# Kernel tuning notes

Hardware: AMD Instinct MI355X
Metric: run time of the kernel (lower is better)

Reference implementation:

```python
import jax, jax.numpy as jnp
import numpy as np

EPS = 1e-5  # torch BatchNorm1d default eps

def _bn(x, g, b):
    # BatchNorm1d in training mode: batch mean, biased variance
    m = jnp.mean(x, axis=0)
    v = jnp.mean((x - m) ** 2, axis=0)
    return g * (x - m) * jax.lax.rsqrt(v + EPS) + b

N_ENT, N_REL = 50000, 200
D_E = D_R = 32
RANK = 32
NI = 1024  # must satisfy NI**2 == D_R * D_E**3
B = 64

def setup_inputs() -> dict:
    key = jax.random.key(0)
    ks = jax.random.split(key, 10)
    s = 0.001
    inp = {
        "E": s * jax.random.normal(ks[0], (N_ENT, D_E), jnp.float32),
        "R": s * jax.random.normal(ks[1], (N_REL, D_R), jnp.float32),
        "U_root": s * jax.random.normal(ks[2], (N_REL, RANK, RANK), jnp.float32),
        "U12": s * jax.random.normal(ks[3], (RANK, NI, NI), jnp.float32),
        "U3R": s * jax.random.normal(ks[4], (RANK, NI, NI), jnp.float32),
        "P": s * jax.random.normal(ks[5], (RANK, D_E), jnp.float32),
        "g_r": jnp.ones((D_R,), jnp.float32), "b_r": jnp.zeros((D_R,), jnp.float32),
        "g_e": jnp.ones((D_E,), jnp.float32), "b_e": jnp.zeros((D_E,), jnp.float32),
        "g_w": jnp.ones((D_E,), jnp.float32), "b_w": jnp.zeros((D_E,), jnp.float32),
        "r_idx": jax.random.randint(ks[6], (B,), 0, N_REL),
        "e2_idx": jax.random.randint(ks[7], (B,), 0, N_ENT),
        "e3_idx": jax.random.randint(ks[8], (B,), 0, N_ENT),
        "miss_ent_domain": 3,
    }
    return inp

def reference(E, R, U_root, U12, U3R, P, g_r, b_r, g_e, b_e, g_w, b_w,
              r_idx, e2_idx, e3_idx, miss_ent_domain):
    Bsz = r_idx.shape[0]
    d_r, d_e = R.shape[1], E.shape[1]

    r_emb = _bn(R[r_idx], g_r, b_r)                      # (B, d_r)

    # einsum 'brs,ria,rjb,rkc->bijk' with P.unsqueeze(1): the dangling
    # indices s, a, b, c are each summed out independently, so the
    # contraction factorizes into rank-1 pieces over r.
    a = U_root[r_idx].sum(-1)                            # (B, r)
    u12 = U12.sum(-1)                                    # (r, ni)
    u3 = U3R.sum(-1)                                     # (r, ni)
    p = P.sum(-1)                                        # (r,)
    W = jnp.einsum('br,ri,rj,r->bij', a, u12, u3, p)     # (B, ni, ni)
    W = W.reshape(Bsz, d_r, d_e, d_e, d_e)               # implicit HT core

    # bmm(r_emb (B,1,d_r), W (B,d_r,-1))
    W_mat = jnp.einsum('bd,bdijk->bijk', r_emb, W)       # (B, d_e, d_e, d_e)

    e2 = _bn(E[e2_idx], g_e, b_e)                        # (B, d_e)
    e3 = _bn(E[e3_idx], g_e, b_e)                        # (B, d_e)

    if miss_ent_domain == 1:
        vec = jnp.einsum('bijk,bk,bj->bi', W_mat, e3, e2)
    elif miss_ent_domain == 2:
        vec = jnp.einsum('bijk,bk,bi->bj', W_mat, e3, e2)
    else:
        vec = jnp.einsum('bijk,bi,bj->bk', W_mat, e2, e3)

    vec = _bn(vec, g_w, b_w)                             # (B, d_e)
    logits = vec @ E.T                                   # (B, |E|)
    return jax.nn.softmax(logits, axis=1)
```

## Files before the change

kernel.cpp:

```cpp
#include <hip/hip_runtime.h>
#include <math.h>

#define NENT 50000
#define DD   32
#define BSZ  64
#define NI   1024
#define NROWS 65536
#define EPS  1e-5f

#define WS_U12S 0
#define WS_U3S  32768
#define WS_P    65536
#define WS_A    65568
#define WS_RE   67616
#define WS_E2   69664
#define WS_E3   71712
#define WS_VEC  73760
#define WS_VECN 75808
#define WS_INV  77856

__device__ void bn_block(const float* __restrict__ src, const int* __restrict__ idx,
                         const float* __restrict__ g, const float* __restrict__ bb,
                         float* __restrict__ dst, float* xs, float* st) {
    for (int i = threadIdx.x; i < BSZ * DD; i += 256) {
        int b = i >> 5, d = i & 31;
        xs[i] = src[(size_t)idx[b] * DD + d];
    }
    __syncthreads();
    if (threadIdx.x < DD) {
        int d = threadIdx.x;
        float m = 0.f;
        for (int b = 0; b < BSZ; ++b) m += xs[b * 32 + d];
        m *= (1.f / 64.f);
        float v = 0.f;
        for (int b = 0; b < BSZ; ++b) { float t = xs[b * 32 + d] - m; v += t * t; }
        v *= (1.f / 64.f);
        st[d]      = m;
        st[32 + d] = g[d] / sqrtf(v + EPS);
    }
    __syncthreads();
    for (int i = threadIdx.x; i < BSZ * DD; i += 256) {
        int d = i & 31;
        dst[i] = (xs[i] - st[d]) * st[32 + d] + bb[d];
    }
    __syncthreads();
}

__global__ __launch_bounds__(256) void k1_rowsums(
    const float* __restrict__ U12, const float* __restrict__ U3R,
    const float* __restrict__ R, const float* __restrict__ E,
    const float* __restrict__ U_root, const float* __restrict__ P,
    const float* __restrict__ g_r, const float* __restrict__ b_r,
    const float* __restrict__ g_e, const float* __restrict__ b_e,
    const int* __restrict__ r_idx, const int* __restrict__ e2_idx,
    const int* __restrict__ e3_idx, float* __restrict__ ws) {
    __shared__ float xs[BSZ * DD];
    __shared__ float st[64];
    int blk = blockIdx.x;
    if (blk < NROWS / 4) {
        int wave = threadIdx.x >> 6, lane = threadIdx.x & 63;
        int row = blk * 4 + wave;
        const float* src = (row < 32768) ? (U12 + (size_t)row * NI)
                                         : (U3R + (size_t)(row - 32768) * NI);
        const float4* p4 = (const float4*)src;
        float s = 0.f;
#pragma unroll
        for (int t = 0; t < 4; ++t) {
            float4 v = p4[t * 64 + lane];
            s += (v.x + v.y) + (v.z + v.w);
        }
#pragma unroll
        for (int o = 32; o; o >>= 1) s += __shfl_down(s, o, 64);
        if (lane == 0) ws[row] = s;
        return;
    }
    int tid = threadIdx.x;
    float* wp   = ws + WS_P;
    float* wa   = ws + WS_A;
    float* wvec = ws + WS_VEC;
    if (tid < 32) {
        float s = 0.f;
#pragma unroll
        for (int c = 0; c < 32; ++c) s += P[tid * 32 + c];
        wp[tid] = s;
    }
    for (int i = tid; i < BSZ * DD; i += 256) {
        int b = i >> 5, r = i & 31;
        const float* u = U_root + (size_t)r_idx[b] * (DD * DD) + r * 32;
        float s = 0.f;
#pragma unroll
        for (int c = 0; c < 32; ++c) s += u[c];
        wa[i]   = s;
        wvec[i] = 0.f;
    }
    bn_block(R, r_idx,  g_r, b_r, ws + WS_RE, xs, st);
    bn_block(E, e2_idx, g_e, b_e, ws + WS_E2, xs, st);
    bn_block(E, e3_idx, g_e, b_e, ws + WS_E3, xs, st);
}

__global__ __launch_bounds__(256) void k2b_core(float* __restrict__ ws) {
    const float* u12s = ws + WS_U12S;
    const float* u3s  = ws + WS_U3S;
    const float* wp   = ws + WS_P;
    const float* wa   = ws + WS_A;
    const float* wre  = ws + WS_RE;
    const float* we2  = ws + WS_E2;
    const float* we3  = ws + WS_E3;
    float* wvec = ws + WS_VEC;
    int lane = threadIdx.x & 63;
    int pair = blockIdx.x * 4 + (threadIdx.x >> 6);
    int b = pair >> 5, r = pair & 31;
    float e2v = we2[b * 32 + (lane & 31)];
    const float* u12r = u12s + r * NI;
    float acc = 0.f;
#pragma unroll
    for (int t = 0; t < 16; ++t) {
        int di = t * 64 + lane;
        acc += u12r[di] * wre[b * 32 + (di >> 5)] * e2v;
    }
#pragma unroll
    for (int o = 32; o; o >>= 1) acc += __shfl_xor(acc, o, 64);
    int k = lane & 31, j0 = (lane >> 5) * 16;
    const float* u3r = u3s + r * NI;
    float bacc = 0.f;
#pragma unroll
    for (int jj = 0; jj < 16; ++jj) {
        int j = j0 + jj;
        bacc += we3[b * 32 + j] * u3r[j * 32 + k];
    }
    bacc += __shfl_down(bacc, 32, 64);
    if (lane < 32) {
        float coef = wa[b * 32 + r] * wp[r] * acc;
        atomicAdd(&wvec[b * 32 + k], coef * bacc);
    }
}

__global__ __launch_bounds__(256) void k2c_bnw(const float* __restrict__ g_w,
                                               const float* __restrict__ b_w,
                                               float* __restrict__ ws) {
    __shared__ float xs[BSZ * DD];
    __shared__ float st[64];
    const float* wvec = ws + WS_VEC;
    float* wvecn = ws + WS_VECN;
    for (int i = threadIdx.x; i < BSZ * DD; i += 256) xs[i] = wvec[i];
    __syncthreads();
    if (threadIdx.x < DD) {
        int d = threadIdx.x;
        float m = 0.f;
        for (int b = 0; b < BSZ; ++b) m += xs[b * 32 + d];
        m *= (1.f / 64.f);
        float v = 0.f;
        for (int b = 0; b < BSZ; ++b) { float t = xs[b * 32 + d] - m; v += t * t; }
        v *= (1.f / 64.f);
        st[d]      = m;
        st[32 + d] = g_w[d] / sqrtf(v + EPS);
    }
    __syncthreads();
    for (int i = threadIdx.x; i < BSZ * DD; i += 256) {
        int d = i & 31;
        wvecn[i] = (xs[i] - st[d]) * st[32 + d] + b_w[d];
    }
}

__global__ __launch_bounds__(256) void k3a_logits(const float* __restrict__ E,
                                                  const float* __restrict__ ws,
                                                  float* __restrict__ out) {
    __shared__ float vs[BSZ * DD];
    const float* wvecn = ws + WS_VECN;
    for (int i = threadIdx.x; i < BSZ * DD; i += 256) vs[i] = wvecn[i];
    __syncthreads();
    int t = threadIdx.x;
    int n = blockIdx.x * 128 + (t & 127);
    int b0 = (t >> 7) * 32;
    if (n >= NENT) return;
    float4 er[8];
    const float4* ep = (const float4*)(E + (size_t)n * DD);
#pragma unroll
    for (int q = 0; q < 8; ++q) er[q] = ep[q];
    for (int b = b0; b < b0 + 32; ++b) {
        const float4* vp = (const float4*)(vs + b * 32);
        float acc = 0.f;
#pragma unroll
        for (int q = 0; q < 8; ++q) {
            float4 vv = vp[q];
            acc += er[q].x * vv.x + er[q].y * vv.y + er[q].z * vv.z + er[q].w * vv.w;
        }
        out[(size_t)b * NENT + n] = expf(acc);
    }
}

__global__ __launch_bounds__(256) void k3b_sums(const float* __restrict__ out,
                                                float* __restrict__ ws) {
    __shared__ float red[4];
    int b = blockIdx.x;
    const float4* row = (const float4*)(out + (size_t)b * NENT);
    float acc = 0.f;
    for (int i = threadIdx.x; i < NENT / 4; i += 256) {
        float4 v = row[i];
        acc += (v.x + v.y) + (v.z + v.w);
    }
#pragma unroll
    for (int o = 32; o; o >>= 1) acc += __shfl_down(acc, o, 64);
    if ((threadIdx.x & 63) == 0) red[threadIdx.x >> 6] = acc;
    __syncthreads();
    if (threadIdx.x == 0) {
        float s = (red[0] + red[1]) + (red[2] + red[3]);
        ws[WS_INV + b] = 1.0f / s;
    }
}

__global__ __launch_bounds__(256) void k3c_norm(float* __restrict__ out,
                                                const float* __restrict__ ws) {
    int idx = blockIdx.x * 256 + threadIdx.x;
    int b = idx / (NENT / 4);
    float inv = ws[WS_INV + b];
    float4* o = (float4*)out;
    float4 v = o[idx];
    v.x *= inv; v.y *= inv; v.z *= inv; v.w *= inv;
    o[idx] = v;
}

extern "C" void kernel_launch(void* const* d_in, const int* in_sizes, int n_in,
                              void* d_out, int out_size, void* d_ws, size_t ws_size,
                              hipStream_t stream) {
    (void)in_sizes; (void)n_in; (void)out_size; (void)ws_size;
    const float* E      = (const float*)d_in[0];
    const float* R      = (const float*)d_in[1];
    const float* U_root = (const float*)d_in[2];
    const float* U12    = (const float*)d_in[3];
    const float* U3R    = (const float*)d_in[4];
    const float* P      = (const float*)d_in[5];
    const float* g_r    = (const float*)d_in[6];
    const float* b_r    = (const float*)d_in[7];
    const float* g_e    = (const float*)d_in[8];
    const float* b_e    = (const float*)d_in[9];
    const float* g_w    = (const float*)d_in[10];
    const float* b_w    = (const float*)d_in[11];
    const int* r_idx    = (const int*)d_in[12];
    const int* e2_idx   = (const int*)d_in[13];
    const int* e3_idx   = (const int*)d_in[14];
    float* ws  = (float*)d_ws;
    float* out = (float*)d_out;

    k1_rowsums<<<dim3(NROWS / 4 + 1), dim3(256), 0, stream>>>(
        U12, U3R, R, E, U_root, P, g_r, b_r, g_e, b_e, r_idx, e2_idx, e3_idx, ws);
    k2b_core<<<dim3(512), dim3(256), 0, stream>>>(ws);
    k2c_bnw<<<dim3(1), dim3(256), 0, stream>>>(g_w, b_w, ws);
    k3a_logits<<<dim3((NENT + 127) / 128), dim3(256), 0, stream>>>(E, ws, out);
    k3b_sums<<<dim3(BSZ), dim3(256), 0, stream>>>(out, ws);
    k3c_norm<<<dim3((NENT / 4 * BSZ) / 256), dim3(256), 0, stream>>>(out, ws);
}
```

Before: 367.6 us.

## Fuse final batchnorm and softmax row sums into logits kernel, batch row-sum loads

Folds the output batchnorm into the logits kernel, where each block recomputes it in shared memory. The logits kernel also accumulates each batch row's exp sums through wave reductions and global atomics, which removes the separate pass that re-read the full output. Separately, the U12/U3R row-sum stage now has each wave reduce 8 rows with more loads in flight, cutting the block count. The cost is redundant BN work in every logits block and many atomics into 64 addresses, and the softmax now uses the fast __expf.

```diff
diff --git a/kernel.cpp b/kernel.cpp
--- a/kernel.cpp
+++ b/kernel.cpp
@@ -16,8 +16,7 @@
 #define WS_E2   69664
 #define WS_E3   71712
 #define WS_VEC  73760
-#define WS_VECN 75808
-#define WS_INV  77856
+#define WS_SUM  75808
 
 __device__ void bn_block(const float* __restrict__ src, const int* __restrict__ idx,
                          const float* __restrict__ g, const float* __restrict__ bb,
@@ -57,21 +56,30 @@
     __shared__ float xs[BSZ * DD];
     __shared__ float st[64];
     int blk = blockIdx.x;
-    if (blk < NROWS / 4) {
-        int wave = threadIdx.x >> 6, lane = threadIdx.x & 63;
-        int row = blk * 4 + wave;
-        const float* src = (row < 32768) ? (U12 + (size_t)row * NI)
-                                         : (U3R + (size_t)(row - 32768) * NI);
-        const float4* p4 = (const float4*)src;
-        float s = 0.f;
-#pragma unroll
-        for (int t = 0; t < 4; ++t) {
-            float4 v = p4[t * 64 + lane];
-            s += (v.x + v.y) + (v.z + v.w);
+    if (blk < 2048) {
+        int w = blk * 4 + (threadIdx.x >> 6);
+        int lane = threadIdx.x & 63;
+        const float* base = (w < 4096) ? U12 : U3R;
+        size_t lrow0 = (w < 4096) ? (size_t)w * 8 : ((size_t)w * 8 - 32768);
+        int grow0 = w * 8;
+        const float4* src = (const float4*)base + lrow0 * 256 + lane;
+#pragma unroll 2
+        for (int p = 0; p < 4; ++p) {
+            const float4* pa = src + (size_t)(2 * p) * 256;
+            float4 a0 = pa[0],   a1 = pa[64],  a2 = pa[128], a3 = pa[192];
+            float4 c0 = pa[256], c1 = pa[320], c2 = pa[384], c3 = pa[448];
+            float sa = ((a0.x + a0.y) + (a0.z + a0.w)) + ((a1.x + a1.y) + (a1.z + a1.w))
+                     + ((a2.x + a2.y) + (a2.z + a2.w)) + ((a3.x + a3.y) + (a3.z + a3.w));
+            float sb = ((c0.x + c0.y) + (c0.z + c0.w)) + ((c1.x + c1.y) + (c1.z + c1.w))
+                     + ((c2.x + c2.y) + (c2.z + c2.w)) + ((c3.x + c3.y) + (c3.z + c3.w));
+            float mine  = (lane < 32) ? sa : sb;
+            float other = __shfl_xor((lane < 32) ? sb : sa, 32, 64);
+            float comb = mine + other;
+#pragma unroll
+            for (int o = 16; o; o >>= 1) comb += __shfl_xor(comb, o, 64);
+            if (lane == 0)  ws[grow0 + 2 * p]     = comb;
+            if (lane == 32) ws[grow0 + 2 * p + 1] = comb;
         }
-#pragma unroll
-        for (int o = 32; o; o >>= 1) s += __shfl_down(s, o, 64);
-        if (lane == 0) ws[row] = s;
         return;
     }
     int tid = threadIdx.x;
@@ -84,6 +92,7 @@
         for (int c = 0; c < 32; ++c) s += P[tid * 32 + c];
         wp[tid] = s;
     }
+    if (tid < 64) ws[WS_SUM + tid] = 0.f;
     for (int i = tid; i < BSZ * DD; i += 256) {
         int b = i >> 5, r = i & 31;
         const float* u = U_root + (size_t)r_idx[b] * (DD * DD) + r * 32;
@@ -135,49 +144,45 @@
     }
 }
 
-__global__ __launch_bounds__(256) void k2c_bnw(const float* __restrict__ g_w,
-                                               const float* __restrict__ b_w,
-                                               float* __restrict__ ws) {
-    __shared__ float xs[BSZ * DD];
+__global__ __launch_bounds__(256) void k3a_logits(const float* __restrict__ E,
+                                                  const float* __restrict__ g_w,
+                                                  const float* __restrict__ b_w,
+                                                  float* __restrict__ ws,
+                                                  float* __restrict__ out) {
+    __shared__ float vs[BSZ * DD];
     __shared__ float st[64];
     const float* wvec = ws + WS_VEC;
-    float* wvecn = ws + WS_VECN;
-    for (int i = threadIdx.x; i < BSZ * DD; i += 256) xs[i] = wvec[i];
-    __syncthreads();
-    if (threadIdx.x < DD) {
-        int d = threadIdx.x;
+    int t = threadIdx.x;
+    for (int i = t; i < BSZ * DD; i += 256) vs[i] = wvec[i];
+    __syncthreads();
+    if (t < DD) {
         float m = 0.f;
-        for (int b = 0; b < BSZ; ++b) m += xs[b * 32 + d];
+        for (int b = 0; b < BSZ; ++b) m += vs[b * 32 + t];
         m *= (1.f / 64.f);
         float v = 0.f;
-        for (int b = 0; b < BSZ; ++b) { float t = xs[b * 32 + d] - m; v += t * t; }
+        for (int b = 0; b < BSZ; ++b) { float d = vs[b * 32 + t] - m; v += d * d; }
         v *= (1.f / 64.f);
-        st[d]      = m;
-        st[32 + d] = g_w[d] / sqrtf(v + EPS);
-    }
-    __syncthreads();
-    for (int i = threadIdx.x; i < BSZ * DD; i += 256) {
+        st[t]      = m;
+        st[32 + t] = g_w[t] / sqrtf(v + EPS);
+    }
+    __syncthreads();
+    for (int i = t; i < BSZ * DD; i += 256) {
         int d = i & 31;
-        wvecn[i] = (xs[i] - st[d]) * st[32 + d] + b_w[d];
-    }
-}
-
-__global__ __launch_bounds__(256) void k3a_logits(const float* __restrict__ E,
-                                                  const float* __restrict__ ws,
-                                                  float* __restrict__ out) {
-    __shared__ float vs[BSZ * DD];
-    const float* wvecn = ws + WS_VECN;
-    for (int i = threadIdx.x; i < BSZ * DD; i += 256) vs[i] = wvecn[i];
-    __syncthreads();
-    int t = threadIdx.x;
-    int n = blockIdx.x * 128 + (t & 127);
+        vs[i] = (vs[i] - st[d]) * st[32 + d] + b_w[d];
+    }
+    __syncthreads();
+    int n  = blockIdx.x * 128 + (t & 127);
     int b0 = (t >> 7) * 32;
-    if (n >= NENT) return;
+    int lane = t & 63;
+    bool valid = n < NENT;
+    int nc = valid ? n : (NENT - 1);
     float4 er[8];
-    const float4* ep = (const float4*)(E + (size_t)n * DD);
+    const float4* ep = (const float4*)(E + (size_t)nc * DD);
 #pragma unroll
     for (int q = 0; q < 8; ++q) er[q] = ep[q];
-    for (int b = b0; b < b0 + 32; ++b) {
+    float* wsum = ws + WS_SUM;
+    for (int j = 0; j < 32; ++j) {
+        int b = b0 + j;
         const float4* vp = (const float4*)(vs + b * 32);
         float acc = 0.f;
 #pragma unroll
@@ -185,27 +190,12 @@
             float4 vv = vp[q];
             acc += er[q].x * vv.x + er[q].y * vv.y + er[q].z * vv.z + er[q].w * vv.w;
         }
-        out[(size_t)b * NENT + n] = expf(acc);
-    }
-}
-
-__global__ __launch_bounds__(256) void k3b_sums(const float* __restrict__ out,
-                                                float* __restrict__ ws) {
-    __shared__ float red[4];
-    int b = blockIdx.x;
-    const float4* row = (const float4*)(out + (size_t)b * NENT);
-    float acc = 0.f;
-    for (int i = threadIdx.x; i < NENT / 4; i += 256) {
-        float4 v = row[i];
-        acc += (v.x + v.y) + (v.z + v.w);
-    }
-#pragma unroll
-    for (int o = 32; o; o >>= 1) acc += __shfl_down(acc, o, 64);
-    if ((threadIdx.x & 63) == 0) red[threadIdx.x >> 6] = acc;
-    __syncthreads();
-    if (threadIdx.x == 0) {
-        float s = (red[0] + red[1]) + (red[2] + red[3]);
-        ws[WS_INV + b] = 1.0f / s;
+        float e = valid ? __expf(acc) : 0.f;
+        if (valid) out[(size_t)b * NENT + n] = e;
+        float s = e;
+#pragma unroll
+        for (int o = 32; o; o >>= 1) s += __shfl_xor(s, o, 64);
+        if (lane == 0) atomicAdd(&wsum[b], s);
     }
 }
 
@@ -213,7 +203,7 @@
                                                 const float* __restrict__ ws) {
     int idx = blockIdx.x * 256 + threadIdx.x;
     int b = idx / (NENT / 4);
-    float inv = ws[WS_INV + b];
+    float inv = 1.0f / ws[WS_SUM + b];
     float4* o = (float4*)out;
     float4 v = o[idx];
     v.x *= inv; v.y *= inv; v.z *= inv; v.w *= inv;
@@ -242,11 +232,9 @@
     float* ws  = (float*)d_ws;
     float* out = (float*)d_out;
 
-    k1_rowsums<<<dim3(NROWS / 4 + 1), dim3(256), 0, stream>>>(
+    k1_rowsums<<<dim3(2049), dim3(256), 0, stream>>>(
         U12, U3R, R, E, U_root, P, g_r, b_r, g_e, b_e, r_idx, e2_idx, e3_idx, ws);
     k2b_core<<<dim3(512), dim3(256), 0, stream>>>(ws);
-    k2c_bnw<<<dim3(1), dim3(256), 0, stream>>>(g_w, b_w, ws);
-    k3a_logits<<<dim3((NENT + 127) / 128), dim3(256), 0, stream>>>(E, ws, out);
-    k3b_sums<<<dim3(BSZ), dim3(256), 0, stream>>>(out, ws);
+    k3a_logits<<<dim3((NENT + 127) / 128), dim3(256), 0, stream>>>(E, g_w, b_w, ws, out);
     k3c_norm<<<dim3((NENT / 4 * BSZ) / 256), dim3(256), 0, stream>>>(out, ws);
 }
```

New measurement: 561.4 us. +52.7%, slower.
